# Kernel tuning notes

Measured on AMD Instinct MI355X. Metric: run time of the kernel, lower is better.

## Reference

```python
import jax, jax.numpy as jnp
import numpy as np
import math

N_HEADS = 8
LN_EPS = 1e-5


def _segment_softmax(att, seg, n):
    # att: [E, H], seg: [E] target-node ids; grouped softmax over edges per target node
    m = jax.ops.segment_max(att, seg, num_segments=n)
    e = jnp.exp(att - m[seg])
    d = jax.ops.segment_sum(e, seg, num_segments=n)
    return e / (d[seg] + 1e-16)


def _layernorm(h, g, b):
    mu = jnp.mean(h, axis=-1, keepdims=True)
    var = jnp.mean((h - mu) ** 2, axis=-1, keepdims=True)
    return (h - mu) * jax.lax.rsqrt(var + LN_EPS) * g + b


def setup_inputs() -> dict:
    key = jax.random.key(0)
    ks = jax.random.split(key, 16)
    T, N, E, Din, Dh = 3, 20000, 100000, 128, 128
    s = 0.02
    x = jax.random.normal(ks[0], (T, N, Din), dtype=jnp.float32)
    edge_index = jax.random.randint(ks[1], (T, 2, E), 0, N, dtype=jnp.int64)
    return {
        "x": x,
        "edge_index": edge_index,
        "Wq": jax.random.normal(ks[2], (Din, Dh), jnp.float32) * s,
        "bq": jnp.zeros((Dh,), jnp.float32),
        "Wk": jax.random.normal(ks[3], (Din, Dh), jnp.float32) * s,
        "bk": jnp.zeros((Dh,), jnp.float32),
        "Wv": jax.random.normal(ks[4], (Din, Dh), jnp.float32) * s,
        "bv": jnp.zeros((Dh,), jnp.float32),
        "ln_g": jnp.ones((Dh,), jnp.float32),
        "ln_b": jnp.zeros((Dh,), jnp.float32),
        "W1": jax.random.normal(ks[5], (Dh, 2 * Dh), jnp.float32) * s,
        "b1": jnp.zeros((2 * Dh,), jnp.float32),
        "W2": jax.random.normal(ks[6], (2 * Dh, Dh), jnp.float32) * s,
        "b2": jnp.zeros((Dh,), jnp.float32),
    }


def reference(x, edge_index, Wq, bq, Wk, bk, Wv, bv, ln_g, ln_b, W1, b1, W2, b2):
    T, N, _ = x.shape
    Dh = Wq.shape[1]
    dk = Dh // N_HEADS
    inv_sqrt_dk = 1.0 / math.sqrt(dk)

    def ffn(h):
        r = _layernorm(h, ln_g, ln_b)
        r = jax.nn.gelu(r @ W1 + b1, approximate=False)
        r = r @ W2 + b2
        return h + r

    xs, cs, ss = [], [], []
    for t_tar in range(T):
        x_tar = x[t_tar]  # [N, Din]
        # collect edges of times 0..t_tar
        tgt = jnp.concatenate([edge_index[t, 1] for t in range(t_tar + 1)])  # [Ec]
        x_tar_e = x_tar[tgt]  # [Ec, Din]
        x_src_e = jnp.concatenate(
            [x[t][edge_index[t, 0]] for t in range(t_tar + 1)], axis=0
        )  # [Ec, Din]

        q = (x_tar_e @ Wq + bq).reshape(-1, N_HEADS, dk)
        k = (x_src_e @ Wk + bk).reshape(-1, N_HEADS, dk)
        v = (x_src_e @ Wv + bv).reshape(-1, N_HEADS, dk)
        att = jnp.sum(q * k, axis=-1) * inv_sqrt_dk  # [Ec, H]

        res_att = _segment_softmax(att, tgt, N)
        spu_att = _segment_softmax(-att, tgt, N)
        res = (v * res_att[..., None]).reshape(-1, Dh)
        spu = (v * spu_att[..., None]).reshape(-1, Dh)
        causal_hat = jax.ops.segment_sum(res, tgt, num_segments=N)
        spurious_hat = jax.ops.segment_sum(spu, tgt, num_segments=N)

        causal = ffn(causal_hat + x_tar)
        spurious = ffn(spurious_hat)
        xs.append(causal + spurious)
        cs.append(causal)
        ss.append(spurious)
    return (jnp.stack(xs), jnp.stack(cs), jnp.stack(ss))
```

## Files before the change

kernel.cpp:

```cpp
#include <hip/hip_runtime.h>
#include <hip/hip_bf16.h>

#define DEV_INLINE __device__ __forceinline__

namespace {

constexpr int T = 3;
constexpr int NN = 20000;
constexpr int NE = 100000;
constexpr int D = 128;
constexpr int D2 = 256;
constexpr int NROW = T * NN;
constexpr size_t OUTSZ = (size_t)T * NN * D;
constexpr int NTILE = T * (NN / 16);

typedef __attribute__((ext_vector_type(8))) short bf16x8;
typedef __attribute__((ext_vector_type(4))) float f32x4;
typedef __attribute__((ext_vector_type(2))) _Float16 h2;
typedef __hip_bfloat16 bf16;

DEV_INLINE unsigned short f2bf(float f) {
  __hip_bfloat16 t = __float2bfloat16(f);
  return *(unsigned short*)&t;
}
DEV_INLINE float bf2f(unsigned short u) { return __uint_as_float((unsigned)u << 16); }

__global__ void k_detect(const unsigned int* __restrict__ ei32, int* __restrict__ flag) {
  int nz = 0;
  for (int i = threadIdx.x; i < 4096; i += 256)
    nz |= (ei32[2 * i + 1] != 0u);
  if (__any(nz) && (threadIdx.x & 63) == 0) atomicOr(&flag[0], 1);
}

DEV_INLINE int loadIdx(const void* ei, int is32, long long idx) {
  return is32 ? ((const int*)ei)[idx] : (int)((const long long*)ei)[idx];
}

__global__ void k_count_precast(
    const void* __restrict__ ei, const int* __restrict__ flag, int* __restrict__ counts,
    const float* __restrict__ Wq, const float* __restrict__ Wk,
    const float* __restrict__ Wv, const float* __restrict__ W1,
    const float* __restrict__ W2, bf16* __restrict__ WqkvT, bf16* __restrict__ W1L,
    bf16* __restrict__ W2L) {
  int i = blockIdx.x * blockDim.x + threadIdx.x;
  int stride = gridDim.x * blockDim.x;
  if (i < T * NE) {
    int is32 = flag[0];
    int t = i / NE, e = i - t * NE;
    int tgt = loadIdx(ei, is32, (long long)(t * 2 + 1) * NE + e);
    atomicAdd(&counts[t * NN + tgt], 1);
  }
  for (int j = i; j < 384 * 128; j += stride) {
    int c = j >> 7, k = j & 127;
    float v = c < 128 ? Wq[k * D + c]
                      : (c < 256 ? Wk[k * D + (c - 128)] : Wv[k * D + (c - 256)]);
    WqkvT[c * 128 + k] = __float2bfloat16(v);
  }
  for (int idx = i; idx < 4 * 256 * 32; idx += stride) {
    int j = idx & 31, c = (idx >> 5) & 255, kk = idx >> 13;
    W1L[idx] = __float2bfloat16(W1[(kk * 32 + j) * D2 + c]);
  }
  for (int idx = i; idx < 8 * 128 * 32; idx += stride) {
    int j = idx & 31, c = (idx >> 5) & 127, kk = idx >> 12;
    W2L[idx] = __float2bfloat16(W2[(kk * 32 + j) * D + c]);
  }
}

__global__ void k_scan(const int* __restrict__ counts, int* __restrict__ offsets,
                       int* __restrict__ cursor) {
  int t = blockIdx.x;
  const int* c = counts + t * NN;
  int* o = offsets + t * (NN + 1);
  int* cur = cursor + t * NN;
  __shared__ int part[256];
  int tid = threadIdx.x;
  constexpr int CH = (NN + 255) / 256;
  int b = tid * CH;
  int e = min(b + CH, NN);
  int s = 0;
  for (int i = b; i < e; i++) s += c[i];
  part[tid] = s;
  __syncthreads();
  for (int d = 1; d < 256; d <<= 1) {
    int v = (tid >= d) ? part[tid - d] : 0;
    __syncthreads();
    part[tid] += v;
    __syncthreads();
  }
  int run = part[tid] - s;
  for (int i = b; i < e; i++) { o[i] = run; cur[i] = run; run += c[i]; }
  if (tid == 255) o[NN] = part[255];
}

__global__ void k_scatter(const void* __restrict__ ei, const int* __restrict__ flag,
                          int* __restrict__ cursor, int* __restrict__ elist) {
  int i = blockIdx.x * blockDim.x + threadIdx.x;
  if (i >= T * NE) return;
  int is32 = flag[0];
  int t = i / NE, e = i - t * NE;
  int src = loadIdx(ei, is32, (long long)(t * 2 + 0) * NE + e);
  int tgt = loadIdx(ei, is32, (long long)(t * 2 + 1) * NE + e);
  int pos = atomicAdd(&cursor[t * NN + tgt], 1);
  elist[t * NE + pos] = src;
}

__global__ __launch_bounds__(256) void k_qkv_mfma(
    const float* __restrict__ x, const bf16* __restrict__ WqkvT,
    const float* __restrict__ bq, const float* __restrict__ bk,
    const float* __restrict__ bv,
    _Float16* __restrict__ Qh, uint2* __restrict__ KV) {
  __shared__ char As[64 * 256];
  __shared__ char Bs[384 * 80];
  int row0 = blockIdx.x * 64;
  int tid = threadIdx.x;
  for (int i = tid; i < 64 * 16; i += 256) {
    int rr = i >> 4, kb = i & 15;
    int grow = row0 + rr;
    uint4 v = make_uint4(0, 0, 0, 0);
    if (grow < NROW) {
      float4 lo = *(const float4*)&x[(size_t)grow * D + kb * 8];
      float4 hi = *(const float4*)&x[(size_t)grow * D + kb * 8 + 4];
      v.x = ((unsigned)f2bf(lo.y) << 16) | f2bf(lo.x);
      v.y = ((unsigned)f2bf(lo.w) << 16) | f2bf(lo.z);
      v.z = ((unsigned)f2bf(hi.y) << 16) | f2bf(hi.x);
      v.w = ((unsigned)f2bf(hi.w) << 16) | f2bf(hi.z);
    }
    *(uint4*)(As + rr * 256 + ((kb * 16) ^ ((rr & 7) << 4))) = v;
  }
  int wid = tid >> 6, lane = tid & 63;
  int lr = lane & 15, lg = lane >> 4;
  f32x4 acc[24];
#pragma unroll
  for (int i = 0; i < 24; i++) acc[i] = (f32x4){0.f, 0.f, 0.f, 0.f};
  for (int kk = 0; kk < 4; kk++) {
    __syncthreads();
    for (int i = tid; i < 384 * 4; i += 256) {
      int c = i >> 2, ko = (i & 3) * 8;
      *(uint4*)(Bs + c * 80 + ko * 2) =
          *(const uint4*)&WqkvT[(size_t)c * 128 + kk * 32 + ko];
    }
    __syncthreads();
    int ar = wid * 16 + lr;
    bf16x8 a = *(bf16x8*)(As + ar * 256 + ((kk * 64 + lg * 16) ^ ((ar & 7) << 4)));
#pragma unroll
    for (int nt = 0; nt < 24; nt++) {
      bf16x8 b = *(bf16x8*)(Bs + (nt * 16 + lr) * 80 + lg * 16);
      acc[nt] = __builtin_amdgcn_mfma_f32_16x16x32_bf16(a, b, acc[nt], 0, 0, 0);
    }
  }
#pragma unroll
  for (int nt = 0; nt < 8; nt++) {
    int c = nt * 16 + lr;
    float bb = bq[c];
#pragma unroll
    for (int j = 0; j < 4; j++) {
      int orow = row0 + wid * 16 + lg * 4 + j;
      if (orow < NROW)
        Qh[(size_t)orow * D + c] = (_Float16)((acc[nt][j] + bb) * 0.25f);
    }
  }
#pragma unroll
  for (int nt = 0; nt < 8; nt++) {
    int c = nt * 16 + lr;
    float bbk = bk[c], bbv = bv[c];
#pragma unroll
    for (int j = 0; j < 4; j++) {
      int orow = row0 + wid * 16 + lg * 4 + j;
      unsigned ku =
          (unsigned)__builtin_bit_cast(unsigned short, (_Float16)(acc[nt + 8][j] + bbk));
      unsigned vu =
          (unsigned)__builtin_bit_cast(unsigned short, (_Float16)(acc[nt + 16][j] + bbv));
      unsigned kn = __shfl_xor(ku, 1, 64);
      unsigned vn = __shfl_xor(vu, 1, 64);
      if ((lr & 1) == 0 && orow < NROW)
        KV[(size_t)orow * 64 + (c >> 1)] = make_uint2((kn << 16) | ku, (vn << 16) | vu);
    }
  }
}

DEV_INLINE float waveReduceSum(float v) {
#pragma unroll
  for (int m = 1; m < 64; m <<= 1) v += __shfl_xor(v, m, 64);
  return v;
}

template <int TS, bool TAIL>
DEV_INLINE void procPair(uint4 kv, const h2* q01, const h2* q23, float* dr, float* ds,
                         float (*ar)[4], float (*as)[4], float valid) {
  h2 k01 = __builtin_bit_cast(h2, kv.x);
  h2 v01 = __builtin_bit_cast(h2, kv.y);
  h2 k23 = __builtin_bit_cast(h2, kv.z);
  h2 v23 = __builtin_bit_cast(h2, kv.w);
  float v0 = (float)v01[0], v1 = (float)v01[1];
  float v2 = (float)v23[0], v3 = (float)v23[1];
#pragma unroll
  for (int tt = TS; tt < 3; tt++) {
    float a = __builtin_amdgcn_fdot2(q23[tt], k23, 0.f, false);
    a = __builtin_amdgcn_fdot2(q01[tt], k01, a, false);
    a += __shfl_xor(a, 1, 64);
    a += __shfl_xor(a, 2, 64);
    float e = __expf(a), f = __expf(-a);
    if (TAIL) { e *= valid; f *= valid; }
    dr[tt] += e; ds[tt] += f;
    ar[tt][0] += e * v0; ar[tt][1] += e * v1;
    ar[tt][2] += e * v2; ar[tt][3] += e * v3;
    as[tt][0] += f * v0; as[tt][1] += f * v1;
    as[tt][2] += f * v2; as[tt][3] += f * v3;
  }
}

__global__ __launch_bounds__(256) void k_attn(
    const _Float16* __restrict__ Qh, const uint2* __restrict__ KV,
    const float* __restrict__ x, const int* __restrict__ offsets,
    const int* __restrict__ elist, const float* __restrict__ lng,
    const float* __restrict__ lnb, bf16* __restrict__ hB, bf16* __restrict__ rb) {
  int n = blockIdx.x * 4 + (threadIdx.x >> 6);
  int l = threadIdx.x & 63;
  int sl = l & 31, half = l >> 5;
  h2 q01[3], q23[3];
#pragma unroll
  for (int tt = 0; tt < 3; tt++) {
    uint2 qu = *(const uint2*)&Qh[((size_t)tt * NN + n) * D + 4 * sl];
    q01[tt] = __builtin_bit_cast(h2, qu.x);
    q23[tt] = __builtin_bit_cast(h2, qu.y);
  }
  float dr[3] = {0.f, 0.f, 0.f}, ds[3] = {0.f, 0.f, 0.f};
  float ar[3][4] = {{0.f}}, as[3][4] = {{0.f}};
#define TSEC(TT)                                                              \
  {                                                                           \
    const int* off = offsets + TT * (NN + 1);                                 \
    int b = off[n], e = off[n + 1];                                           \
    const int* el = elist + TT * NE;                                          \
    const uint2* KVt = KV + (size_t)TT * NN * 64;                             \
    int i = b;                                                                \
    for (; i + 4 <= e; i += 4) {                                              \
      int s0 = el[i + half];                                                  \
      int s1 = el[i + 2 + half];                                              \
      uint4 kv0 = *(const uint4*)&KVt[(size_t)s0 * 64 + 2 * sl];              \
      uint4 kv1 = *(const uint4*)&KVt[(size_t)s1 * 64 + 2 * sl];              \
      procPair<TT, false>(kv0, q01, q23, dr, ds, ar, as, 1.f);                \
      procPair<TT, false>(kv1, q01, q23, dr, ds, ar, as, 1.f);                \
    }                                                                         \
    for (; i + 2 <= e; i += 2) {                                              \
      int s = el[i + half];                                                   \
      uint4 kv = *(const uint4*)&KVt[(size_t)s * 64 + 2 * sl];                \
      procPair<TT, false>(kv, q01, q23, dr, ds, ar, as, 1.f);                 \
    }                                                                         \
    if (i < e) {                                                              \
      int s = el[i];                                                          \
      uint4 kv = *(const uint4*)&KVt[(size_t)s * 64 + 2 * sl];                \
      procPair<TT, true>(kv, q01, q23, dr, ds, ar, as, half ? 0.f : 1.f);     \
    }                                                                         \
  }
  TSEC(0)
  TSEC(1)
  TSEC(2)
#undef TSEC
#pragma unroll
  for (int tt = 0; tt < 3; tt++) {
    dr[tt] += __shfl_xor(dr[tt], 32, 64);
    ds[tt] += __shfl_xor(ds[tt], 32, 64);
#pragma unroll
    for (int d4 = 0; d4 < 4; d4++) {
      ar[tt][d4] += __shfl_xor(ar[tt][d4], 32, 64);
      as[tt][d4] += __shfl_xor(as[tt][d4], 32, 64);
    }
  }
  float4 g4 = *(const float4*)&lng[4 * sl];
  float4 b4 = *(const float4*)&lnb[4 * sl];
#pragma unroll
  for (int tt = 0; tt < 3; tt++) {
    float4 xr = *(const float4*)&x[((size_t)tt * NN + n) * D + 4 * sl];
    float ir = 1.f / (dr[tt] + 1e-16f), is = 1.f / (ds[tt] + 1e-16f);
    float hc[4], hs[4];
    hc[0] = ar[tt][0] * ir + xr.x;
    hc[1] = ar[tt][1] * ir + xr.y;
    hc[2] = ar[tt][2] * ir + xr.z;
    hc[3] = ar[tt][3] * ir + xr.w;
#pragma unroll
    for (int j = 0; j < 4; j++) hs[j] = as[tt][j] * is;
    float mu = waveReduceSum(hc[0] + hc[1] + hc[2] + hc[3]) * (1.f / 256.f);
    float dx[4], ss = 0.f;
#pragma unroll
    for (int j = 0; j < 4; j++) { dx[j] = hc[j] - mu; ss += dx[j] * dx[j]; }
    float var = waveReduceSum(ss) * (1.f / 256.f);
    float rstd = rsqrtf(var + 1e-5f);
    float rc[4];
    rc[0] = dx[0] * rstd * g4.x + b4.x;
    rc[1] = dx[1] * rstd * g4.y + b4.y;
    rc[2] = dx[2] * rstd * g4.z + b4.z;
    rc[3] = dx[3] * rstd * g4.w + b4.w;
    float mu2 = waveReduceSum(hs[0] + hs[1] + hs[2] + hs[3]) * (1.f / 256.f);
    float ex[4], ss2 = 0.f;
#pragma unroll
    for (int j = 0; j < 4; j++) { ex[j] = hs[j] - mu2; ss2 += ex[j] * ex[j]; }
    float var2 = waveReduceSum(ss2) * (1.f / 256.f);
    float rstd2 = rsqrtf(var2 + 1e-5f);
    float rs[4];
    rs[0] = ex[0] * rstd2 * g4.x + b4.x;
    rs[1] = ex[1] * rstd2 * g4.y + b4.y;
    rs[2] = ex[2] * rstd2 * g4.z + b4.z;
    rs[3] = ex[3] * rstd2 * g4.w + b4.w;
    if (half == 0) {
      size_t base = (size_t)tt * 2 * NN;
      size_t iC = (base + n) * D + 4 * sl;
      size_t iS = (base + NN + n) * D + 4 * sl;
      *(uint2*)&hB[iC] = make_uint2(((unsigned)f2bf(hc[1]) << 16) | f2bf(hc[0]),
                                    ((unsigned)f2bf(hc[3]) << 16) | f2bf(hc[2]));
      *(uint2*)&hB[iS] = make_uint2(((unsigned)f2bf(hs[1]) << 16) | f2bf(hs[0]),
                                    ((unsigned)f2bf(hs[3]) << 16) | f2bf(hs[2]));
      *(uint2*)&rb[iC] = make_uint2(((unsigned)f2bf(rc[1]) << 16) | f2bf(rc[0]),
                                    ((unsigned)f2bf(rc[3]) << 16) | f2bf(rc[2]));
      *(uint2*)&rb[iS] = make_uint2(((unsigned)f2bf(rs[1]) << 16) | f2bf(rs[0]),
                                    ((unsigned)f2bf(rs[3]) << 16) | f2bf(rs[2]));
    }
  }
}

__global__ __launch_bounds__(512) void k_ffn_fused(
    const bf16* __restrict__ rb, const bf16* __restrict__ W1L,
    const bf16* __restrict__ W2L, const float* __restrict__ b1,
    const float* __restrict__ b2, const bf16* __restrict__ h,
    float* __restrict__ out) {
  __shared__ char As[32 * 256];
  __shared__ char Gs[32 * 528];
  int tid = threadIdx.x;
  int wid = tid >> 6, lane = tid & 63;
  int lr = lane & 15, lg = lane >> 4;
  int wr = (wid & 1) * 16;
  int wc1 = (wid >> 1) * 64;
  int wc2 = (wid >> 1) * 32;
  int ar = wr + lr;
  bf16x8 w1f[4][4];
#pragma unroll
  for (int kk = 0; kk < 4; kk++)
#pragma unroll
    for (int nt = 0; nt < 4; nt++)
      w1f[kk][nt] =
          *(const bf16x8*)&W1L[((size_t)kk * 256 + wc1 + nt * 16 + lr) * 32 + lg * 8];
  bf16x8 w2f[8][2];
#pragma unroll
  for (int kk = 0; kk < 8; kk++)
#pragma unroll
    for (int nt = 0; nt < 2; nt++)
      w2f[kk][nt] =
          *(const bf16x8*)&W2L[((size_t)kk * 128 + wc2 + nt * 16 + lr) * 32 + lg * 8];
  float bb1[4], bb2[2];
#pragma unroll
  for (int nt = 0; nt < 4; nt++) bb1[nt] = b1[wc1 + nt * 16 + lr];
#pragma unroll
  for (int nt = 0; nt < 2; nt++) bb2[nt] = b2[wc2 + nt * 16 + lr];
  int srr = tid >> 4, skb = tid & 15;
  int tile = blockIdx.x;
  uint4 pref;
  {
    int t2 = tile / 1250, nb = tile - t2 * 1250;
    size_t grow = (size_t)t2 * 2 * NN + (size_t)(srr & 1) * NN + nb * 16 + (srr >> 1);
    pref = *(const uint4*)&rb[grow * D + skb * 8];
  }
  for (; tile < NTILE; tile += gridDim.x) {
    int t2 = tile / 1250, nb = tile - t2 * 1250;
    int n0 = nb * 16;
    size_t base = (size_t)t2 * 2 * NN;
    *(uint4*)(As + srr * 256 + ((skb * 16) ^ ((srr & 7) << 4))) = pref;
    float hpref[2][4];
#pragma unroll
    for (int nt = 0; nt < 2; nt++) {
      int c = wc2 + nt * 16 + lr;
#pragma unroll
      for (int j = 0; j < 4; j++) {
        int rr2 = wr + lg * 4 + j;
        hpref[nt][j] = bf2f(*(const unsigned short*)&h[
            (base + (size_t)(rr2 & 1) * NN + n0 + (rr2 >> 1)) * D + c]);
      }
    }
    int ntile = tile + gridDim.x;
    if (ntile < NTILE) {
      int t2n = ntile / 1250, nbn = ntile - t2n * 1250;
      size_t grow =
          (size_t)t2n * 2 * NN + (size_t)(srr & 1) * NN + nbn * 16 + (srr >> 1);
      pref = *(const uint4*)&rb[grow * D + skb * 8];
    }
    __syncthreads();
    f32x4 acc1[4];
#pragma unroll
    for (int i = 0; i < 4; i++) acc1[i] = (f32x4){0.f, 0.f, 0.f, 0.f};
#pragma unroll
    for (int kk = 0; kk < 4; kk++) {
      bf16x8 a = *(bf16x8*)(As + ar * 256 + ((kk * 64 + lg * 16) ^ ((ar & 7) << 4)));
#pragma unroll
      for (int nt = 0; nt < 4; nt++)
        acc1[nt] =
            __builtin_amdgcn_mfma_f32_16x16x32_bf16(a, w1f[kk][nt], acc1[nt], 0, 0, 0);
    }
#pragma unroll
    for (int nt = 0; nt < 4; nt++) {
      int c = wc1 + nt * 16 + lr;
#pragma unroll
      for (int j = 0; j < 4; j++) {
        int r = wr + lg * 4 + j;
        float y = acc1[nt][j] + bb1[nt];
        y = 0.5f * y * (1.f + erff(y * 0.70710678118654752f));
        unsigned us = f2bf(y);
        unsigned nbv = __shfl_xor(us, 1, 64);
        if ((lr & 1) == 0) *(unsigned*)(Gs + r * 528 + c * 2) = (nbv << 16) | us;
      }
    }
    __syncthreads();
    f32x4 acc2[2];
#pragma unroll
    for (int i = 0; i < 2; i++) acc2[i] = (f32x4){0.f, 0.f, 0.f, 0.f};
#pragma unroll
    for (int kk = 0; kk < 8; kk++) {
      bf16x8 a = *(bf16x8*)(Gs + ar * 528 + kk * 64 + lg * 16);
#pragma unroll
      for (int nt = 0; nt < 2; nt++)
        acc2[nt] =
            __builtin_amdgcn_mfma_f32_16x16x32_bf16(a, w2f[kk][nt], acc2[nt], 0, 0, 0);
    }
#pragma unroll
    for (int nt = 0; nt < 2; nt++) {
      int c = wc2 + nt * 16 + lr;
      float z[4];
#pragma unroll
      for (int j = 0; j < 4; j++) z[j] = acc2[nt][j] + bb2[nt] + hpref[nt][j];
#pragma unroll
      for (int m = 0; m < 2; m++) {
        int node = n0 + ((wr + lg * 4) >> 1) + m;
        size_t oidx = ((size_t)t2 * NN + node) * D + c;
        out[OUTSZ + oidx] = z[2 * m];
        out[2 * OUTSZ + oidx] = z[2 * m + 1];
        out[oidx] = z[2 * m] + z[2 * m + 1];
      }
    }
  }
}

}

extern "C" void kernel_launch(void* const* d_in, const int* in_sizes, int n_in,
                              void* d_out, int out_size, void* d_ws, size_t ws_size,
                              hipStream_t stream) {
  const float* x = (const float*)d_in[0];
  const void* ei = d_in[1];
  const float* Wq = (const float*)d_in[2];
  const float* bq = (const float*)d_in[3];
  const float* Wk = (const float*)d_in[4];
  const float* bk = (const float*)d_in[5];
  const float* Wv = (const float*)d_in[6];
  const float* bv = (const float*)d_in[7];
  const float* lng = (const float*)d_in[8];
  const float* lnb = (const float*)d_in[9];
  const float* W1 = (const float*)d_in[10];
  const float* b1 = (const float*)d_in[11];
  const float* W2 = (const float*)d_in[12];
  const float* b2 = (const float*)d_in[13];
  float* out = (float*)d_out;

  char* ws = (char*)d_ws;
  size_t off = 0;
  auto alloc = [&](size_t bytes) -> void* {
    void* p = ws + off;
    off += (bytes + 255) & ~(size_t)255;
    return p;
  };
  bf16* WqkvT = (bf16*)alloc((size_t)384 * 128 * 2);
  bf16* W1L = (bf16*)alloc((size_t)128 * 256 * 2);
  bf16* W2L = (bf16*)alloc((size_t)256 * 128 * 2);
  _Float16* Qh = (_Float16*)alloc((size_t)NROW * D * 2);
  uint2* KV = (uint2*)alloc((size_t)NROW * 64 * 8);
  bf16* hB = (bf16*)alloc((size_t)T * 2 * NN * D * 2);
  bf16* rb = (bf16*)alloc((size_t)T * 2 * NN * D * 2);
  int* counts = (int*)alloc((size_t)T * NN * 4);
  int* offsets = (int*)alloc((size_t)T * (NN + 1) * 4);
  int* cursor = (int*)alloc((size_t)T * NN * 4);
  int* elist = (int*)alloc((size_t)T * NE * 4);
  int* dflag = (int*)alloc(256);

  hipMemsetAsync(counts, 0, (size_t)T * NN * 4, stream);
  hipMemsetAsync(dflag, 0, 8, stream);
  k_detect<<<1, 256, 0, stream>>>((const unsigned int*)ei, dflag);
  int eb = (T * NE + 255) / 256;
  k_count_precast<<<eb, 256, 0, stream>>>(ei, dflag, counts, Wq, Wk, Wv, W1, W2,
                                          WqkvT, W1L, W2L);
  k_scan<<<T, 256, 0, stream>>>(counts, offsets, cursor);
  k_scatter<<<eb, 256, 0, stream>>>(ei, dflag, cursor, elist);
  k_qkv_mfma<<<(NROW + 63) / 64, 256, 0, stream>>>(x, WqkvT, bq, bk, bv, Qh, KV);
  k_attn<<<NN / 4, 256, 0, stream>>>(Qh, KV, x, offsets, elist, lng, lnb, hB, rb);
  k_ffn_fused<<<512, 512, 0, stream>>>(rb, W1L, W2L, b1, b2, hB, out);
}
```

Baseline: 243.1 us.

## Fuse edge scatter into QKV kernel, unroll attention loop, use tanh-form GELU

Merges the edge scatter into the QKV GEMM kernel as a grid-stride prologue, removing one launch. Widens the attention edge loop from 4 to 8 edges per iteration to keep more KV gathers in flight. Replaces exact erf GELU with the tanh-form approximation written through an exp, and doubles the FFN grid size. The GELU change alters numerics slightly, and the atomic scatter now delays the GEMM work inside each block.

```diff
diff --git a/kernel.cpp b/kernel.cpp
--- a/kernel.cpp
+++ b/kernel.cpp
@@ -24,6 +24,11 @@
   return *(unsigned short*)&t;
 }
 DEV_INLINE float bf2f(unsigned short u) { return __uint_as_float((unsigned)u << 16); }
+
+DEV_INLINE float gelu_fast(float y) {
+  float y3 = y * y * y;
+  return y / (1.f + __expf(-1.5957691216f * (y + 0.044715f * y3)));
+}
 
 __global__ void k_detect(const unsigned int* __restrict__ ei32, int* __restrict__ flag) {
   int nz = 0;
@@ -92,27 +97,28 @@
   if (tid == 255) o[NN] = part[255];
 }
 
-__global__ void k_scatter(const void* __restrict__ ei, const int* __restrict__ flag,
-                          int* __restrict__ cursor, int* __restrict__ elist) {
-  int i = blockIdx.x * blockDim.x + threadIdx.x;
-  if (i >= T * NE) return;
-  int is32 = flag[0];
-  int t = i / NE, e = i - t * NE;
-  int src = loadIdx(ei, is32, (long long)(t * 2 + 0) * NE + e);
-  int tgt = loadIdx(ei, is32, (long long)(t * 2 + 1) * NE + e);
-  int pos = atomicAdd(&cursor[t * NN + tgt], 1);
-  elist[t * NE + pos] = src;
-}
-
 __global__ __launch_bounds__(256) void k_qkv_mfma(
     const float* __restrict__ x, const bf16* __restrict__ WqkvT,
     const float* __restrict__ bq, const float* __restrict__ bk,
-    const float* __restrict__ bv,
-    _Float16* __restrict__ Qh, uint2* __restrict__ KV) {
+    const float* __restrict__ bv, _Float16* __restrict__ Qh, uint2* __restrict__ KV,
+    const void* __restrict__ ei, const int* __restrict__ flag,
+    int* __restrict__ cursor, int* __restrict__ elist) {
   __shared__ char As[64 * 256];
   __shared__ char Bs[384 * 80];
   int row0 = blockIdx.x * 64;
   int tid = threadIdx.x;
+  {
+    int gid = blockIdx.x * 256 + tid;
+    int gstride = gridDim.x * 256;
+    int is32 = flag[0];
+    for (int i2 = gid; i2 < T * NE; i2 += gstride) {
+      int t = i2 / NE, e2 = i2 - t * NE;
+      int src = loadIdx(ei, is32, (long long)(t * 2 + 0) * NE + e2);
+      int tgt = loadIdx(ei, is32, (long long)(t * 2 + 1) * NE + e2);
+      int pos = atomicAdd(&cursor[t * NN + tgt], 1);
+      elist[t * NE + pos] = src;
+    }
+  }
   for (int i = tid; i < 64 * 16; i += 256) {
     int rr = i >> 4, kb = i & 15;
     int grow = row0 + rr;
@@ -233,13 +239,19 @@
     const int* el = elist + TT * NE;                                          \
     const uint2* KVt = KV + (size_t)TT * NN * 64;                             \
     int i = b;                                                                \
-    for (; i + 4 <= e; i += 4) {                                              \
+    for (; i + 8 <= e; i += 8) {                                              \
       int s0 = el[i + half];                                                  \
       int s1 = el[i + 2 + half];                                              \
+      int s2 = el[i + 4 + half];                                              \
+      int s3 = el[i + 6 + half];                                              \
       uint4 kv0 = *(const uint4*)&KVt[(size_t)s0 * 64 + 2 * sl];              \
       uint4 kv1 = *(const uint4*)&KVt[(size_t)s1 * 64 + 2 * sl];              \
+      uint4 kv2 = *(const uint4*)&KVt[(size_t)s2 * 64 + 2 * sl];              \
+      uint4 kv3 = *(const uint4*)&KVt[(size_t)s3 * 64 + 2 * sl];              \
       procPair<TT, false>(kv0, q01, q23, dr, ds, ar, as, 1.f);                \
       procPair<TT, false>(kv1, q01, q23, dr, ds, ar, as, 1.f);                \
+      procPair<TT, false>(kv2, q01, q23, dr, ds, ar, as, 1.f);                \
+      procPair<TT, false>(kv3, q01, q23, dr, ds, ar, as, 1.f);                \
     }                                                                         \
     for (; i + 2 <= e; i += 2) {                                              \
       int s = el[i + half];                                                   \
@@ -399,8 +411,7 @@
 #pragma unroll
       for (int j = 0; j < 4; j++) {
         int r = wr + lg * 4 + j;
-        float y = acc1[nt][j] + bb1[nt];
-        y = 0.5f * y * (1.f + erff(y * 0.70710678118654752f));
+        float y = gelu_fast(acc1[nt][j] + bb1[nt]);
         unsigned us = f2bf(y);
         unsigned nbv = __shfl_xor(us, 1, 64);
         if ((lr & 1) == 0) *(unsigned*)(Gs + r * 528 + c * 2) = (nbv << 16) | us;
@@ -484,8 +495,8 @@
   k_count_precast<<<eb, 256, 0, stream>>>(ei, dflag, counts, Wq, Wk, Wv, W1, W2,
                                           WqkvT, W1L, W2L);
   k_scan<<<T, 256, 0, stream>>>(counts, offsets, cursor);
-  k_scatter<<<eb, 256, 0, stream>>>(ei, dflag, cursor, elist);
-  k_qkv_mfma<<<(NROW + 63) / 64, 256, 0, stream>>>(x, WqkvT, bq, bk, bv, Qh, KV);
+  k_qkv_mfma<<<(NROW + 63) / 64, 256, 0, stream>>>(x, WqkvT, bq, bk, bv, Qh, KV, ei,
+                                                   dflag, cursor, elist);
   k_attn<<<NN / 4, 256, 0, stream>>>(Qh, KV, x, offsets, elist, lng, lnb, hB, rb);
-  k_ffn_fused<<<512, 512, 0, stream>>>(rb, W1L, W2L, b1, b2, hB, out);
-}
+  k_ffn_fused<<<1024, 512, 0, stream>>>(rb, W1L, W2L, b1, b2, hB, out);
+}
```

After: 252.1 us. +3.7%, slower.
